# Kernel optimization log

Hardware: AMD Instinct MI355X
Metric: run time of the kernel (lower is better)

## Reference

```python
import jax, jax.numpy as jnp
import numpy as np

N_NODES = 100000
N_EDGES = 600000
N_GRAPHS = 64


def _segment_mean(x, seg_ids, num_segments):
    s = jax.ops.segment_sum(x, seg_ids, num_segments=num_segments)
    cnt = jax.ops.segment_sum(jnp.ones((x.shape[0],), x.dtype), seg_ids, num_segments=num_segments)
    return s / jnp.maximum(cnt, 1.0)[:, None]


def _sage_conv(x, src, dst, W_l, W_r, b):
    # PyG SAGEConv (mean aggr): out = lin_l(mean_{j->i} x_j) + lin_r(x_i)
    mean_nb = _segment_mean(x[src], dst, x.shape[0])  # [N, d_in]
    return mean_nb @ W_l.T + x @ W_r.T + b


def setup_inputs() -> dict:
    key = jax.random.key(0)
    ks = jax.random.split(key, 16)
    bert_cls = jax.random.normal(ks[0], (N_GRAPHS, 768), jnp.float32)
    node_x = jax.random.normal(ks[1], (N_NODES, 128), jnp.float32)
    edge_index = jax.random.randint(ks[2], (2, N_EDGES), 0, N_NODES, jnp.int64 if jax.config.jax_enable_x64 else jnp.int32)
    batch_ids = jnp.sort(jax.random.randint(ks[3], (N_NODES,), 0, N_GRAPHS))
    s = 0.05
    return {
        'bert_cls': bert_cls,
        'node_x': node_x,
        'edge_index': edge_index,
        'batch_ids': batch_ids,
        'W_adapt': jax.random.normal(ks[4], (64, 768), jnp.float32) * s,
        'b_adapt': jnp.zeros((64,), jnp.float32),
        'W1l': jax.random.normal(ks[5], (64, 128), jnp.float32) * s,
        'W1r': jax.random.normal(ks[6], (64, 128), jnp.float32) * s,
        'b1': jnp.zeros((64,), jnp.float32),
        'W2l': jax.random.normal(ks[7], (16, 64), jnp.float32) * s,
        'W2r': jax.random.normal(ks[8], (16, 64), jnp.float32) * s,
        'b2': jnp.zeros((16,), jnp.float32),
        'Wm': jax.random.normal(ks[9], (16, 16), jnp.float32) * s,
        'bm': jnp.zeros((16,), jnp.float32),
    }


def reference(bert_cls, node_x, edge_index, batch_ids,
              W_adapt, b_adapt, W1l, W1r, b1, W2l, W2r, b2, Wm, bm):
    # pooled BERT CLS -> adaptive linear (forward() applies no relu here)
    last_state = bert_cls @ W_adapt.T + b_adapt  # [bs, 64]

    src, dst = edge_index[0], edge_index[1]
    h = jax.nn.relu(_sage_conv(node_x, src, dst, W1l, W1r, b1))  # [N, 64]
    h = _sage_conv(h, src, dst, W2l, W2r, b2)                    # [N, 16]

    graph_emb = _segment_mean(h, batch_ids, N_GRAPHS)            # [bs, 16]
    graph_emb = graph_emb @ Wm.T + bm

    return jnp.concatenate([last_state, graph_emb], axis=-1)     # [bs, 80]
```

## Files before the change

### kernel.cpp

```cpp
#include <hip/hip_runtime.h>

#define N_NODES 100000
#define N_EDGES 600000
#define N_GRAPHS 64


__global__ void k_count(const int* __restrict__ dst, int* __restrict__ deg) {
    int e = blockIdx.x * 256 + threadIdx.x;
    if (e < N_EDGES) atomicAdd(&deg[dst[e]], 1);
}

__global__ void k_scan1(const int* __restrict__ deg, int* __restrict__ offs,
                        int* __restrict__ bsums) {
    __shared__ int s[256];
    int t = threadIdx.x, b = blockIdx.x;
    int base = b * 1024 + t * 4;
    int v0 = (base + 0 < N_NODES) ? deg[base + 0] : 0;
    int v1 = (base + 1 < N_NODES) ? deg[base + 1] : 0;
    int v2 = (base + 2 < N_NODES) ? deg[base + 2] : 0;
    int v3 = (base + 3 < N_NODES) ? deg[base + 3] : 0;
    int tsum = v0 + v1 + v2 + v3;
    s[t] = tsum;
    __syncthreads();
    for (int o = 1; o < 256; o <<= 1) {
        int x = (t >= o) ? s[t - o] : 0;
        __syncthreads();
        s[t] += x;
        __syncthreads();
    }
    int p = s[t] - tsum;
    if (base + 0 < N_NODES) offs[base + 0] = p;
    p += v0;
    if (base + 1 < N_NODES) offs[base + 1] = p;
    p += v1;
    if (base + 2 < N_NODES) offs[base + 2] = p;
    p += v2;
    if (base + 3 < N_NODES) offs[base + 3] = p;
    if (t == 255) bsums[b] = s[255];
}

__global__ void k_scan2(const int* __restrict__ bsums, int* __restrict__ boff) {
    __shared__ int s[128];
    int t = threadIdx.x;
    int nb = (N_NODES + 1023) / 1024;
    int v = (t < nb) ? bsums[t] : 0;
    s[t] = v;
    __syncthreads();
    for (int o = 1; o < 128; o <<= 1) {
        int x = (t >= o) ? s[t - o] : 0;
        __syncthreads();
        s[t] += x;
        __syncthreads();
    }
    boff[t] = s[t] - v;
}

__global__ void k_scan3(int* __restrict__ offs, const int* __restrict__ boff,
                        int* __restrict__ cursor) {
    int i = blockIdx.x * 256 + threadIdx.x;
    if (i < N_NODES) {
        int v = offs[i] + boff[i >> 10];
        offs[i] = v;
        cursor[i] = v;
    }
}

__global__ void k_fill(const int* __restrict__ src, const int* __restrict__ dst,
                       int* __restrict__ cursor, int* __restrict__ ssrc) {
    int e = blockIdx.x * 256 + threadIdx.x;
    if (e < N_EDGES) {
        int d = dst[e];
        int pos = atomicAdd(&cursor[d], 1);
        ssrc[pos] = src[e];
    }
}

__global__ void k_prepack(const float* __restrict__ W1l, const float* __restrict__ W1r,
                          const float* __restrict__ W2l, const float* __restrict__ W2r,
                          float2* __restrict__ P) {
    int i = blockIdx.x * 256 + threadIdx.x;
    if (i < 4096) {
        int m = i >> 6, d = i & 63;
        P[i] = make_float2(W1l[d * 128 + 2 * m], W1l[d * 128 + 2 * m + 1]);
    } else if (i < 8192) {
        int j = i - 4096, m = j >> 6, d = j & 63;
        P[i] = make_float2(W1r[d * 128 + 2 * m], W1r[d * 128 + 2 * m + 1]);
    } else if (i < 8704) {
        int j = i - 8192, m = j >> 4, d = j & 15;
        P[i] = make_float2(W2l[d * 64 + 2 * m], W2l[d * 64 + 2 * m + 1]);
    } else if (i < 9216) {
        int j = i - 8704, m = j >> 4, d = j & 15;
        P[i] = make_float2(W2r[d * 64 + 2 * m], W2r[d * 64 + 2 * m + 1]);
    }
}


__launch_bounds__(256)
__global__ void k_xform1(const float* __restrict__ x,
                         const float2* __restrict__ Pl, const float2* __restrict__ Pr,
                         float* __restrict__ xl, float* __restrict__ xr) {
    __shared__ float2 S[64 * 64];
    int tid = threadIdx.x;
    int wave = __builtin_amdgcn_readfirstlane(tid >> 6);
    int lane = tid & 63;
    int tbase = blockIdx.x * 64;
    const float4* x4 = (const float4*)x;

    for (int idx = tid; idx < 64 * 32; idx += 256) {
        int n = idx >> 5, m4 = idx & 31;
        if (tbase + n < N_NODES) {
            float4 v = x4[(tbase + n) * 32 + m4];
            int swz = n & 31;
            S[n * 64 + ((2 * m4) ^ swz)]     = make_float2(v.x, v.y);
            S[n * 64 + ((2 * m4 + 1) ^ swz)] = make_float2(v.z, v.w);
        }
    }
    __syncthreads();

    int node = tbase + lane;
    int dbase = wave * 16;
    float accl[16], accr[16];
#pragma unroll
    for (int dd = 0; dd < 16; ++dd) { accl[dd] = 0.f; accr[dd] = 0.f; }
    int swz = lane & 31;
    const float2* Sn = S + lane * 64;
#pragma unroll 4
    for (int m = 0; m < 64; ++m) {
        float2 s = Sn[m ^ swz];
        const float2* Wl = Pl + m * 64 + dbase;
        const float2* Wr = Pr + m * 64 + dbase;
#pragma unroll
        for (int dd = 0; dd < 16; ++dd) {
            accl[dd] = fmaf(Wl[dd].x, s.x, fmaf(Wl[dd].y, s.y, accl[dd]));
            accr[dd] = fmaf(Wr[dd].x, s.x, fmaf(Wr[dd].y, s.y, accr[dd]));
        }
    }
    if (node < N_NODES) {
        float4* pl = (float4*)(xl + node * 64 + dbase);
        float4* pr = (float4*)(xr + node * 64 + dbase);
#pragma unroll
        for (int p = 0; p < 4; ++p) {
            pl[p] = make_float4(accl[4 * p], accl[4 * p + 1], accl[4 * p + 2], accl[4 * p + 3]);
            pr[p] = make_float4(accr[4 * p], accr[4 * p + 1], accr[4 * p + 2], accr[4 * p + 3]);
        }
    }
}


__launch_bounds__(256)
__global__ void k_gather1(const float* __restrict__ xl, const int* __restrict__ ssrc,
                          const int* __restrict__ offs, const int* __restrict__ deg,
                          const float* __restrict__ b1, float* __restrict__ h1) {
    int tid = blockIdx.x * 256 + threadIdx.x;
    int wid = tid >> 6, lane = tid & 63;
    int nWaves = (gridDim.x * 256) >> 6;
    float bias = b1[lane];

    for (int node = wid; node < N_NODES; node += nWaves) {
        int o  = __builtin_amdgcn_readfirstlane(offs[node]);
        int dg = __builtin_amdgcn_readfirstlane(deg[node]);
        float self = h1[node * 64 + lane];
        float a0 = 0.f, a1 = 0.f, a2 = 0.f, a3 = 0.f;
        int last = dg - 1;
        for (int u = 0; u < dg; u += 4) {
            int n0 = ssrc[o + u];
            int n1 = ssrc[o + min(u + 1, last)];
            int n2 = ssrc[o + min(u + 2, last)];
            int n3 = ssrc[o + min(u + 3, last)];
            float v0 = xl[n0 * 64 + lane];
            float v1 = xl[n1 * 64 + lane];
            float v2 = xl[n2 * 64 + lane];
            float v3 = xl[n3 * 64 + lane];
            float m1 = (u + 1 < dg) ? 1.f : 0.f;
            float m2 = (u + 2 < dg) ? 1.f : 0.f;
            float m3 = (u + 3 < dg) ? 1.f : 0.f;
            a0 += v0;
            a1 = fmaf(v1, m1, a1);
            a2 = fmaf(v2, m2, a2);
            a3 = fmaf(v3, m3, a3);
        }
        float inv = 1.f / (float)max(dg, 1);
        h1[node * 64 + lane] = fmaxf(self + bias + ((a0 + a1) + (a2 + a3)) * inv, 0.f);
    }
}


__launch_bounds__(256)
__global__ void k_xform2(const float* __restrict__ h1,
                         const float2* __restrict__ Pl, const float2* __restrict__ Pr,
                         float* __restrict__ h1l, float* __restrict__ h2pre) {
    __shared__ float2 S[64 * 32];
    int tid = threadIdx.x;
    int wave = __builtin_amdgcn_readfirstlane(tid >> 6);
    int lane = tid & 63;
    int tbase = blockIdx.x * 64;
    const float4* h4 = (const float4*)h1;

    for (int idx = tid; idx < 64 * 16; idx += 256) {
        int n = idx >> 4, m4 = idx & 15;
        if (tbase + n < N_NODES) {
            float4 v = h4[(tbase + n) * 16 + m4];
            int swz = n & 31;
            S[n * 32 + ((2 * m4) ^ swz)]     = make_float2(v.x, v.y);
            S[n * 32 + ((2 * m4 + 1) ^ swz)] = make_float2(v.z, v.w);
        }
    }
    __syncthreads();

    int node = tbase + lane;
    int dbase = wave * 4;
    float accl[4] = {0.f, 0.f, 0.f, 0.f};
    float accr[4] = {0.f, 0.f, 0.f, 0.f};
    int swz = lane & 31;
    const float2* Sn = S + lane * 32;
#pragma unroll 4
    for (int m = 0; m < 32; ++m) {
        float2 s = Sn[m ^ swz];
        const float2* Wl = Pl + m * 16 + dbase;
        const float2* Wr = Pr + m * 16 + dbase;
#pragma unroll
        for (int dd = 0; dd < 4; ++dd) {
            accl[dd] = fmaf(Wl[dd].x, s.x, fmaf(Wl[dd].y, s.y, accl[dd]));
            accr[dd] = fmaf(Wr[dd].x, s.x, fmaf(Wr[dd].y, s.y, accr[dd]));
        }
    }
    if (node < N_NODES) {
        *(float4*)(h1l + node * 16 + dbase)   = make_float4(accl[0], accl[1], accl[2], accl[3]);
        *(float4*)(h2pre + node * 16 + dbase) = make_float4(accr[0], accr[1], accr[2], accr[3]);
    }
}


__launch_bounds__(256)
__global__ void k_g2pool(const float* __restrict__ h1l, const float* __restrict__ h2pre,
                         const int* __restrict__ ssrc, const int* __restrict__ offs,
                         const int* __restrict__ deg, const int* __restrict__ batch,
                         const float* __restrict__ b2,
                         float* __restrict__ gsum, float* __restrict__ gcnt) {
    __shared__ float bins[N_GRAPHS][17];
    int tid = threadIdx.x;
    for (int i = tid; i < N_GRAPHS * 17; i += 256) ((float*)bins)[i] = 0.f;
    __syncthreads();

    int wave = tid >> 6, lane = tid & 63;
    int sub = lane >> 4, d = lane & 15;
    float bias = b2[d];

    int chunk = (N_NODES + gridDim.x - 1) / gridDim.x;
    int cs = blockIdx.x * chunk;
    int ce = min(N_NODES, cs + chunk);

    for (int base = cs + wave * 4; base < ce; base += 16) {
        int node = base + sub;
        bool valid = node < ce;
        int nn = valid ? node : cs;
        int o = offs[nn], dg = deg[nn];
        float a0 = 0.f, a1 = 0.f, a2 = 0.f, a3 = 0.f;
        int last = dg - 1;
        for (int u = 0; u < dg; u += 4) {
            int n0 = ssrc[o + u];
            int n1 = ssrc[o + min(u + 1, last)];
            int n2 = ssrc[o + min(u + 2, last)];
            int n3 = ssrc[o + min(u + 3, last)];
            float v0 = h1l[n0 * 16 + d];
            float v1 = h1l[n1 * 16 + d];
            float v2 = h1l[n2 * 16 + d];
            float v3 = h1l[n3 * 16 + d];
            float m1 = (u + 1 < dg) ? 1.f : 0.f;
            float m2 = (u + 2 < dg) ? 1.f : 0.f;
            float m3 = (u + 3 < dg) ? 1.f : 0.f;
            a0 += v0;
            a1 = fmaf(v1, m1, a1);
            a2 = fmaf(v2, m2, a2);
            a3 = fmaf(v3, m3, a3);
        }
        float inv = 1.f / (float)max(dg, 1);
        float val = h2pre[nn * 16 + d] + bias + ((a0 + a1) + (a2 + a3)) * inv;
        if (valid) {
            int g = batch[nn];
            atomicAdd(&bins[g][d], val);
            if (d == 0) atomicAdd(&bins[g][16], 1.f);
        }
    }
    __syncthreads();
    for (int i = tid; i < N_GRAPHS * 17; i += 256) {
        int g = i / 17, c = i - g * 17;
        float v = bins[g][c];
        if (v != 0.f) {
            if (c < 16) atomicAdd(&gsum[g * 16 + c], v);
            else        atomicAdd(&gcnt[g], v);
        }
    }
}


__global__ void k_final(const float* __restrict__ bert, const float* __restrict__ Wad,
                        const float* __restrict__ bad, const float* __restrict__ Wm,
                        const float* __restrict__ bm, const float* __restrict__ gsum,
                        const float* __restrict__ gcnt, float* __restrict__ out) {
    int g = blockIdx.x;
    int t = threadIdx.x;
    if (t < 64) {
        const float4* br = (const float4*)(bert + g * 768);
        const float4* wr = (const float4*)(Wad + t * 768);
        float acc = bad[t];
#pragma unroll 8
        for (int k = 0; k < 192; ++k) {
            float4 bv = br[k], wv = wr[k];
            acc += bv.x * wv.x + bv.y * wv.y + bv.z * wv.z + bv.w * wv.w;
        }
        out[g * 80 + t] = acc;
    } else if (t < 80) {
        int j = t - 64;
        float ic = 1.f / fmaxf(gcnt[g], 1.f);
        float acc = bm[j];
#pragma unroll
        for (int k = 0; k < 16; ++k) acc += Wm[j * 16 + k] * gsum[g * 16 + k] * ic;
        out[g * 80 + t] = acc;
    }
}

extern "C" void kernel_launch(void* const* d_in, const int* in_sizes, int n_in,
                              void* d_out, int out_size, void* d_ws, size_t ws_size,
                              hipStream_t stream) {
    const float* bert   = (const float*)d_in[0];
    const float* node_x = (const float*)d_in[1];
    const int*   edge   = (const int*)d_in[2];
    const int*   batch  = (const int*)d_in[3];
    const float* Wad    = (const float*)d_in[4];
    const float* bad    = (const float*)d_in[5];
    const float* W1l    = (const float*)d_in[6];
    const float* W1r    = (const float*)d_in[7];
    const float* b1     = (const float*)d_in[8];
    const float* W2l    = (const float*)d_in[9];
    const float* W2r    = (const float*)d_in[10];
    const float* b2     = (const float*)d_in[11];
    const float* Wm     = (const float*)d_in[12];
    const float* bm     = (const float*)d_in[13];
    float* out = (float*)d_out;

    const int* src = edge;
    const int* dst = edge + N_EDGES;

    char* ws = (char*)d_ws;
    int*    deg    = (int*)(ws);
    int*    offs   = (int*)(ws + 400000);
    int*    cursor = (int*)(ws + 800000);
    int*    bsums  = (int*)(ws + 1200000);
    int*    boff   = (int*)(ws + 1200512);
    int*    ssrc   = (int*)(ws + 1201024);
    float*  xl     = (float*)(ws + 3601024);
    float*  h1     = (float*)(ws + 29201024);
    float2* P      = (float2*)(ws + 54801024);
    float*  gsum   = (float*)(ws + 54874752);
    float*  gcnt   = (float*)(ws + 54878848);
    float*  h1l    = (float*)(ws + 3601024);
    float*  h2pre  = (float*)(ws + 10001024);

    float2* P1l = P;
    float2* P1r = P + 4096;
    float2* P2l = P + 8192;
    float2* P2r = P + 8704;

    hipMemsetAsync(deg, 0, 400000, stream);
    hipMemsetAsync(gsum, 0, 4096 + 256, stream);

    k_count<<<(N_EDGES + 255) / 256, 256, 0, stream>>>(dst, deg);
    k_scan1<<<(N_NODES + 1023) / 1024, 256, 0, stream>>>(deg, offs, bsums);
    k_scan2<<<1, 128, 0, stream>>>(bsums, boff);
    k_scan3<<<(N_NODES + 255) / 256, 256, 0, stream>>>(offs, boff, cursor);
    k_fill<<<(N_EDGES + 255) / 256, 256, 0, stream>>>(src, dst, cursor, ssrc);
    k_prepack<<<36, 256, 0, stream>>>(W1l, W1r, W2l, W2r, P);

    int nTiles = (N_NODES + 63) / 64;
    k_xform1<<<nTiles, 256, 0, stream>>>(node_x, P1l, P1r, xl, h1);
    k_gather1<<<2048, 256, 0, stream>>>(xl, ssrc, offs, deg, b1, h1);
    k_xform2<<<nTiles, 256, 0, stream>>>(h1, P2l, P2r, h1l, h2pre);
    k_g2pool<<<512, 256, 0, stream>>>(h1l, h2pre, ssrc, offs, deg, batch, b2, gsum, gcnt);
    k_final<<<N_GRAPHS, 128, 0, stream>>>(bert, Wad, bad, Wm, bm, gsum, gcnt, out);
}
```

Measured before the change: 357.6 us.

## Rewrite layer-1 transform as register-tiled 128x128 GEMM with K-chunked shared tiles

The first-layer node transform becomes a classic register-blocked SGEMM. Each block computes 128 nodes × 128 outputs (the concatenated W1l and W1r), and each thread holds an 8x8 accumulator. Node features and packed weights are staged in shared memory in 32-wide K chunks. This replaces the previous scheme, where each thread did outer products against weights read directly from global memory, and is meant to raise arithmetic intensity and cut global weight traffic. In exchange it uses more registers (64 accumulators), needs two syncs per chunk, and writes transposed shared-memory stores that may cause bank conflicts.

Result: faster. 325.2 us (-9.0%).

```diff
diff --git a/kernel.cpp b/kernel.cpp
--- a/kernel.cpp
+++ b/kernel.cpp
@@ -77,71 +77,86 @@
 
 __global__ void k_prepack(const float* __restrict__ W1l, const float* __restrict__ W1r,
                           const float* __restrict__ W2l, const float* __restrict__ W2r,
-                          float2* __restrict__ P) {
+                          float* __restrict__ Pg, float2* __restrict__ P2) {
     int i = blockIdx.x * 256 + threadIdx.x;
-    if (i < 4096) {
-        int m = i >> 6, d = i & 63;
-        P[i] = make_float2(W1l[d * 128 + 2 * m], W1l[d * 128 + 2 * m + 1]);
-    } else if (i < 8192) {
-        int j = i - 4096, m = j >> 6, d = j & 63;
-        P[i] = make_float2(W1r[d * 128 + 2 * m], W1r[d * 128 + 2 * m + 1]);
-    } else if (i < 8704) {
-        int j = i - 8192, m = j >> 4, d = j & 15;
-        P[i] = make_float2(W2l[d * 64 + 2 * m], W2l[d * 64 + 2 * m + 1]);
-    } else if (i < 9216) {
-        int j = i - 8704, m = j >> 4, d = j & 15;
-        P[i] = make_float2(W2r[d * 64 + 2 * m], W2r[d * 64 + 2 * m + 1]);
-    }
-}
-
-
-__launch_bounds__(256)
-__global__ void k_xform1(const float* __restrict__ x,
-                         const float2* __restrict__ Pl, const float2* __restrict__ Pr,
+    if (i < 16384) {
+        int k = i >> 7, d = i & 127;
+        Pg[i] = (d < 64) ? W1l[d * 128 + k] : W1r[(d - 64) * 128 + k];
+    } else if (i < 16896) {
+        int j = i - 16384, m = j >> 4, d = j & 15;
+        P2[j] = make_float2(W2l[d * 64 + 2 * m], W2l[d * 64 + 2 * m + 1]);
+    } else if (i < 17408) {
+        int j = i - 16896, m = j >> 4, d = j & 15;
+        P2[512 + j] = make_float2(W2r[d * 64 + 2 * m], W2r[d * 64 + 2 * m + 1]);
+    }
+}
+
+
+#define KC 32
+#define LDP 132
+
+__launch_bounds__(256, 4)
+__global__ void k_xform1(const float* __restrict__ x, const float* __restrict__ Pg,
                          float* __restrict__ xl, float* __restrict__ xr) {
-    __shared__ float2 S[64 * 64];
+    __shared__ float At[KC * LDP];
+    __shared__ float Bt[KC * LDP];
     int tid = threadIdx.x;
-    int wave = __builtin_amdgcn_readfirstlane(tid >> 6);
-    int lane = tid & 63;
-    int tbase = blockIdx.x * 64;
+    int wave = tid >> 6, lane = tid & 63;
+    int wr = wave >> 1, wc = wave & 1;
+    int li = lane >> 3, lj = lane & 7;
+    int tbase = blockIdx.x * 128;
     const float4* x4 = (const float4*)x;
-
-    for (int idx = tid; idx < 64 * 32; idx += 256) {
-        int n = idx >> 5, m4 = idx & 31;
-        if (tbase + n < N_NODES) {
-            float4 v = x4[(tbase + n) * 32 + m4];
-            int swz = n & 31;
-            S[n * 64 + ((2 * m4) ^ swz)]     = make_float2(v.x, v.y);
-            S[n * 64 + ((2 * m4 + 1) ^ swz)] = make_float2(v.z, v.w);
-        }
-    }
-    __syncthreads();
-
-    int node = tbase + lane;
-    int dbase = wave * 16;
-    float accl[16], accr[16];
-#pragma unroll
-    for (int dd = 0; dd < 16; ++dd) { accl[dd] = 0.f; accr[dd] = 0.f; }
-    int swz = lane & 31;
-    const float2* Sn = S + lane * 64;
+    const float4* Pg4 = (const float4*)Pg;
+
+    float acc[8][8];
+#pragma unroll
+    for (int i = 0; i < 8; ++i)
+#pragma unroll
+        for (int j = 0; j < 8; ++j) acc[i][j] = 0.f;
+
+    for (int k0 = 0; k0 < 128; k0 += KC) {
+        if (k0) __syncthreads();
+#pragma unroll
+        for (int u = 0; u < 4; ++u) {
+            int idx = u * 256 + tid;
+            int n = idx >> 3, q = idx & 7;
+            int node = min(tbase + n, N_NODES - 1);
+            float4 v = x4[node * 32 + (k0 >> 2) + q];
+            At[(4 * q + 0) * LDP + n] = v.x;
+            At[(4 * q + 1) * LDP + n] = v.y;
+            At[(4 * q + 2) * LDP + n] = v.z;
+            At[(4 * q + 3) * LDP + n] = v.w;
+        }
+#pragma unroll
+        for (int u = 0; u < 4; ++u) {
+            int idx = u * 256 + tid;
+            int kk = idx >> 5, q = idx & 31;
+            float4 w = Pg4[(k0 + kk) * 32 + q];
+            *(float4*)&Bt[kk * LDP + 4 * q] = w;
+        }
+        __syncthreads();
 #pragma unroll 4
-    for (int m = 0; m < 64; ++m) {
-        float2 s = Sn[m ^ swz];
-        const float2* Wl = Pl + m * 64 + dbase;
-        const float2* Wr = Pr + m * 64 + dbase;
-#pragma unroll
-        for (int dd = 0; dd < 16; ++dd) {
-            accl[dd] = fmaf(Wl[dd].x, s.x, fmaf(Wl[dd].y, s.y, accl[dd]));
-            accr[dd] = fmaf(Wr[dd].x, s.x, fmaf(Wr[dd].y, s.y, accr[dd]));
-        }
-    }
-    if (node < N_NODES) {
-        float4* pl = (float4*)(xl + node * 64 + dbase);
-        float4* pr = (float4*)(xr + node * 64 + dbase);
-#pragma unroll
-        for (int p = 0; p < 4; ++p) {
-            pl[p] = make_float4(accl[4 * p], accl[4 * p + 1], accl[4 * p + 2], accl[4 * p + 3]);
-            pr[p] = make_float4(accr[4 * p], accr[4 * p + 1], accr[4 * p + 2], accr[4 * p + 3]);
+        for (int kk = 0; kk < KC; ++kk) {
+            float a[8], b[8];
+            *(float4*)&a[0] = *(const float4*)&At[kk * LDP + wr * 64 + li * 8];
+            *(float4*)&a[4] = *(const float4*)&At[kk * LDP + wr * 64 + li * 8 + 4];
+            *(float4*)&b[0] = *(const float4*)&Bt[kk * LDP + wc * 64 + lj * 8];
+            *(float4*)&b[4] = *(const float4*)&Bt[kk * LDP + wc * 64 + lj * 8 + 4];
+#pragma unroll
+            for (int i = 0; i < 8; ++i)
+#pragma unroll
+                for (int j = 0; j < 8; ++j)
+                    acc[i][j] = fmaf(a[i], b[j], acc[i][j]);
+        }
+    }
+    float* outb = wc ? xr : xl;
+#pragma unroll
+    for (int i = 0; i < 8; ++i) {
+        int node = tbase + wr * 64 + li * 8 + i;
+        if (node < N_NODES) {
+            float4* p = (float4*)(outb + node * 64 + lj * 8);
+            p[0] = make_float4(acc[i][0], acc[i][1], acc[i][2], acc[i][3]);
+            p[1] = make_float4(acc[i][4], acc[i][5], acc[i][6], acc[i][7]);
         }
     }
 }
@@ -351,16 +366,15 @@
     int*    ssrc   = (int*)(ws + 1201024);
     float*  xl     = (float*)(ws + 3601024);
     float*  h1     = (float*)(ws + 29201024);
-    float2* P      = (float2*)(ws + 54801024);
+    float*  Pg     = (float*)(ws + 54801024);
+    float2* P2     = (float2*)(ws + 54866560);
     float*  gsum   = (float*)(ws + 54874752);
     float*  gcnt   = (float*)(ws + 54878848);
     float*  h1l    = (float*)(ws + 3601024);
     float*  h2pre  = (float*)(ws + 10001024);
 
-    float2* P1l = P;
-    float2* P1r = P + 4096;
-    float2* P2l = P + 8192;
-    float2* P2r = P + 8704;
+    float2* P2l = P2;
+    float2* P2r = P2 + 512;
 
     hipMemsetAsync(deg, 0, 400000, stream);
     hipMemsetAsync(gsum, 0, 4096 + 256, stream);
@@ -370,12 +384,13 @@
     k_scan2<<<1, 128, 0, stream>>>(bsums, boff);
     k_scan3<<<(N_NODES + 255) / 256, 256, 0, stream>>>(offs, boff, cursor);
     k_fill<<<(N_EDGES + 255) / 256, 256, 0, stream>>>(src, dst, cursor, ssrc);
-    k_prepack<<<36, 256, 0, stream>>>(W1l, W1r, W2l, W2r, P);
-
-    int nTiles = (N_NODES + 63) / 64;
-    k_xform1<<<nTiles, 256, 0, stream>>>(node_x, P1l, P1r, xl, h1);
+    k_prepack<<<68, 256, 0, stream>>>(W1l, W1r, W2l, W2r, Pg, P2);
+
+    int nT128 = (N_NODES + 127) / 128;
+    int nT64  = (N_NODES + 63) / 64;
+    k_xform1<<<nT128, 256, 0, stream>>>(node_x, Pg, xl, h1);
     k_gather1<<<2048, 256, 0, stream>>>(xl, ssrc, offs, deg, b1, h1);
-    k_xform2<<<nTiles, 256, 0, stream>>>(h1, P2l, P2r, h1l, h2pre);
+    k_xform2<<<nT64, 256, 0, stream>>>(h1, P2l, P2r, h1l, h2pre);
     k_g2pool<<<512, 256, 0, stream>>>(h1l, h2pre, ssrc, offs, deg, batch, b2, gsum, gcnt);
     k_final<<<N_GRAPHS, 128, 0, stream>>>(bert, Wad, bad, Wm, bm, gsum, gcnt, out);
 }
```
